# Performance work log

Measured on AMD Instinct MI355X. Metric: run time of the kernel, lower is better.

## Reference

```python
import jax, jax.numpy as jnp
from jax import lax
import numpy as np

B, S = 256, 512
VOCAB, EMB_D = 50000, 300
POS_MAX, POS_D = 512, 16
CNN_OUT, K, NCLASS = 50, 5, 10


def setup_inputs() -> dict:
    key = jax.random.key(0)
    ks = jax.random.split(key, 7)
    return {
        "tokens": jax.random.randint(ks[0], (B, S), 0, VOCAB),
        "embed_table": jax.random.normal(ks[1], (VOCAB, EMB_D), jnp.float32),
        "pos_table": jax.random.normal(ks[2], (POS_MAX, POS_D), jnp.float32),
        "conv_w": jax.random.normal(ks[3], (CNN_OUT, EMB_D + 2 * POS_D, K), jnp.float32) * 0.05,
        "conv_b": jax.random.normal(ks[4], (CNN_OUT,), jnp.float32) * 0.05,
        "fc_w": jax.random.normal(ks[5], (NCLASS, CNN_OUT), jnp.float32) * 0.1,
        "fc_b": jax.random.normal(ks[6], (NCLASS,), jnp.float32) * 0.1,
        "entity1": 1,
        "entity2": 2,
    }


def _nearest_entity_dist(tokens, entity, max_pos):
    # Distance from each token to the nearest occurrence of `entity`,
    # clipped to [0, max_pos-1]; sentences without the entity clip to max.
    Sl = tokens.shape[1]
    idx = jnp.arange(Sl)
    occ = tokens == entity  # [B, S]
    big = 2 * Sl
    # nearest occurrence index to the left (running max) and right (running min)
    left = lax.cummax(jnp.where(occ, idx, -big), axis=1)
    right = lax.cummin(jnp.where(occ, idx, big), axis=1, reverse=True)
    dist = jnp.minimum(idx - left, right - idx)
    return jnp.clip(dist, 0, max_pos - 1)


def reference(tokens, embed_table, pos_table, conv_w, conv_b, fc_w, fc_b,
              entity1, entity2):
    emb = embed_table[tokens]                      # [B, S, EMB_D] gather
    pad = jnp.all(emb == 0.0, axis=-1)             # [B, S] zero-row mask
    feats = [emb]
    for ent in (entity1, entity2):
        d = _nearest_entity_dist(tokens, ent, pos_table.shape[0])
        pe = pos_table[d]                          # [B, S, POS_D]
        pe = jnp.where(pad[..., None], 0.0, pe)    # zero masked positions
        feats.append(pe)
    x = jnp.concatenate(feats, axis=-1)            # [B, S, 332]
    x = jnp.transpose(x, (0, 2, 1))                # [B, C, S]
    pad_hw = conv_w.shape[-1] // 2
    y = lax.conv_general_dilated(
        x, conv_w, window_strides=(1,), padding=[(pad_hw, pad_hw)],
        dimension_numbers=("NCH", "OIH", "NCH"))
    y = jax.nn.relu(y + conv_b[None, :, None])     # [B, 50, S]
    y = jnp.max(y, axis=2)                         # full-length max pool -> [B, 50]
    out = y @ fc_w.T + fc_b                        # [B, NCLASS]
    return out
```

## Files before the change

kernel.cpp:

```cpp
#include <hip/hip_runtime.h>
#include <hip/hip_bf16.h>

typedef __attribute__((ext_vector_type(8))) short short8;
typedef __attribute__((ext_vector_type(4))) float floatx4;

#define BB 256
#define SS 512
#define VOCAB 50000
#define EMB_D 300
#define POS_MAX 512
#define POS_D 16
#define CNN_OUT 50
#define KW 5
#define NCLASS 10
#define C_IN 332
#define KS2 10
#define NB2 20
#define NWF2 (KS2 * NB2 * 64 * 8)
#define PSTR 320
#define ESTR 328
#define FSTR2 328
#define MTOK 32
#define MROWS 64
#define FROWS 68
#define NB_PACK 225
#define NB_POSP 640
#define NB_DIST BB

__device__ __forceinline__ unsigned pack2bf(float x, float y) {
    __hip_bfloat162 h = __float22bfloat162_rn(make_float2(x, y));
    return *reinterpret_cast<unsigned*>(&h);
}

__device__ __forceinline__ unsigned short f2bf(float x) {
    unsigned u = __float_as_uint(x);
    u += 0x7FFF + ((u >> 16) & 1);
    return (unsigned short)(u >> 16);
}

__device__ __forceinline__ float bflo(unsigned u) { return __uint_as_float(u << 16); }
__device__ __forceinline__ float bfhi(unsigned u) { return __uint_as_float(u & 0xFFFF0000u); }

__device__ __forceinline__ unsigned comb(unsigned a, unsigned b, unsigned c,
                                         float sa, float sp) {
    float rlo = sa * bflo(a) + sp * (bflo(b) + bflo(c));
    float rhi = sa * bfhi(a) + sp * (bfhi(b) + bfhi(c));
    return pack2bf(rlo, rhi);
}

__global__ __launch_bounds__(512) void k_prep(const float* __restrict__ conv_w,
                                              const float* __restrict__ pos,
                                              unsigned short* __restrict__ Wf2,
                                              unsigned short* __restrict__ P1,
                                              unsigned short* __restrict__ P2,
                                              float* __restrict__ ymax,
                                              const int* __restrict__ tokens,
                                              const int* __restrict__ e1p,
                                              const int* __restrict__ e2p,
                                              int* __restrict__ d1,
                                              int* __restrict__ d2) {
    __shared__ int cnt1, cnt2;
    __shared__ int lst1[SS], lst2[SS];
    int bid = blockIdx.x, tid = threadIdx.x;
    if (bid < NB_PACK) {
        int idx = bid * 512 + tid;
        if (idx < NWF2) {
            int j = idx & 7, l = (idx >> 3) & 63;
            int rest = idx >> 9;
            int nb = rest % 20, ks = rest / 20;
            int c = ks * 32 + ((l >> 4) << 3) + j;
            int col = nb * 16 + (l & 15);
            int k = col >> 6, o = col & 63;
            float v = 0.f;
            if (c < EMB_D && o < CNN_OUT)
                v = conv_w[o * (C_IN * KW) + c * KW + k];
            Wf2[idx] = f2bf(v);
        } else if (idx < NWF2 + BB * CNN_OUT) {
            ymax[idx - NWF2] = 0.f;
        }
    } else if (bid < NB_PACK + NB_POSP) {
        int idx = (bid - NB_PACK) * 512 + tid;
        int tb = idx / (POS_MAX * PSTR);
        int r = idx % (POS_MAX * PSTR);
        int d = r / PSTR, col = r % PSTR;
        int k = col >> 6, o = col & 63;
        float v = 0.f;
        if (o < CNN_OUT) {
            const float* pr = pos + d * POS_D;
            const float* wb = conv_w + o * (C_IN * KW) + (EMB_D + tb * POS_D) * KW + k;
            #pragma unroll
            for (int c = 0; c < POS_D; ++c) v += pr[c] * wb[c * KW];
        }
        (tb ? P2 : P1)[d * PSTR + col] = f2bf(v);
    } else {
        int b = bid - NB_PACK - NB_POSP;
        int s = tid;
        if (s == 0) { cnt1 = 0; cnt2 = 0; }
        __syncthreads();
        int tok = tokens[b * SS + s];
        int e1 = *e1p, e2 = *e2p;
        if (tok == e1) lst1[atomicAdd(&cnt1, 1)] = s;
        if (tok == e2) lst2[atomicAdd(&cnt2, 1)] = s;
        __syncthreads();
        int dd1 = POS_MAX - 1;
        int n1 = cnt1;
        for (int i = 0; i < n1; ++i) dd1 = min(dd1, abs(s - lst1[i]));
        int dd2 = POS_MAX - 1;
        int n2 = cnt2;
        for (int i = 0; i < n2; ++i) dd2 = min(dd2, abs(s - lst2[i]));
        d1[b * SS + s] = dd1;
        d2[b * SS + s] = dd2;
    }
}

__global__ __launch_bounds__(256, 2) void k_proj(const float* __restrict__ E,
                                                 const unsigned short* __restrict__ Wf2,
                                                 unsigned short* __restrict__ P,
                                                 int* __restrict__ rowz) {
    __shared__ __align__(16) unsigned short Elds[MTOK * ESTR];
    __shared__ int nzf[MTOK];
    int tid = threadIdx.x, lane = tid & 63, w = tid >> 6;
    int t0 = blockIdx.x * MTOK;

    if (tid < MTOK) nzf[tid] = 0;
    __syncthreads();

    float4 v[10];
    int vrow[10], vc4[10];
    bool vok[10];
    #pragma unroll
    for (int j = 0; j < 10; ++j) {
        int idx = tid + j * 256;
        vok[j] = (idx < MTOK * 75);
        int row = idx / 75, c4 = idx - row * 75;
        vrow[j] = row; vc4[j] = c4;
        int t = t0 + row;
        v[j] = (vok[j] && t < VOCAB)
             ? ((const float4*)(E + (size_t)t * EMB_D))[c4]
             : make_float4(0.f, 0.f, 0.f, 0.f);
    }
    #pragma unroll
    for (int j = 0; j < 10; ++j) {
        if (vok[j]) {
            bool nz = (v[j].x != 0.f) | (v[j].y != 0.f) | (v[j].z != 0.f) | (v[j].w != 0.f);
            if (nz) nzf[vrow[j]] = 1;
            *(uint2*)&Elds[vrow[j] * ESTR + vc4[j] * 4] =
                make_uint2(pack2bf(v[j].x, v[j].y), pack2bf(v[j].z, v[j].w));
        }
    }
    if (tid < MTOK * 5) {
        int row = tid / 5, u = tid - row * 5;
        *(uint2*)&Elds[row * ESTR + 300 + u * 4] = make_uint2(0u, 0u);
    }
    __syncthreads();

    if (tid < MTOK) {
        int t = t0 + tid;
        if (t < VOCAB) rowz[t] = nzf[tid] ? 0 : 1;
    }

    floatx4 acc[2][5];
    #pragma unroll
    for (int mm = 0; mm < 2; ++mm)
        #pragma unroll
        for (int nb = 0; nb < 5; ++nb) acc[mm][nb] = (floatx4)0.f;

    int arow = lane & 15, ach = (lane >> 4) * 8;
    const short8* Bp = (const short8*)Wf2;

    short8 bA[5], bB[5];
    #pragma unroll
    for (int nb = 0; nb < 5; ++nb)
        bA[nb] = Bp[(0 * NB2 + w * 5 + nb) * 64 + lane];
    #pragma unroll
    for (int nb = 0; nb < 5; ++nb)
        bB[nb] = Bp[(1 * NB2 + w * 5 + nb) * 64 + lane];

    auto step = [&](int ks, short8 (&bf)[5], int pfks) {
        short8 af[2];
        #pragma unroll
        for (int mm = 0; mm < 2; ++mm)
            af[mm] = *(const short8*)&Elds[(mm * 16 + arow) * ESTR + ks * 32 + ach];
        #pragma unroll
        for (int mm = 0; mm < 2; ++mm)
            #pragma unroll
            for (int nb = 0; nb < 5; ++nb)
                acc[mm][nb] = __builtin_amdgcn_mfma_f32_16x16x32_bf16(af[mm], bf[nb], acc[mm][nb], 0, 0, 0);
        if (pfks < KS2) {
            #pragma unroll
            for (int nb = 0; nb < 5; ++nb)
                bf[nb] = Bp[(pfks * NB2 + w * 5 + nb) * 64 + lane];
        }
    };

    #pragma unroll 1
    for (int ks = 0; ks < KS2; ks += 2) {
        step(ks, bA, ks + 2);
        step(ks + 1, bB, ks + 3);
    }

    __syncthreads();
    int drow = (lane >> 4) * 4, dcol = lane & 15;
    #pragma unroll
    for (int mm = 0; mm < 2; ++mm)
        #pragma unroll
        for (int nb = 0; nb < 5; ++nb)
            #pragma unroll
            for (int rg = 0; rg < 4; ++rg)
                Elds[(mm * 16 + drow + rg) * ESTR + (w * 5 + nb) * 16 + dcol] = f2bf(acc[mm][nb][rg]);
    __syncthreads();
    #pragma unroll
    for (int j = 0; j < 5; ++j) {
        int idx = tid + j * 256;
        int row = idx / 40, ch = idx - row * 40;
        int tt = t0 + row;
        if (tt < VOCAB)
            ((uint4*)P)[(size_t)tt * 40 + ch] = *(const uint4*)&Elds[row * ESTR + ch * 8];
    }
}

__global__ __launch_bounds__(512, 4) void k_conv(const int* __restrict__ tokens,
                                                 const int* __restrict__ d1,
                                                 const int* __restrict__ d2,
                                                 const int* __restrict__ rowz,
                                                 const unsigned short* __restrict__ P,
                                                 const unsigned short* __restrict__ P1,
                                                 const unsigned short* __restrict__ P2,
                                                 const float* __restrict__ conv_b,
                                                 float* __restrict__ ymax) {
    __shared__ __align__(16) unsigned short F[FROWS * FSTR2];
    __shared__ int td[FROWS], i1d[FROWS], i2d[FROWS];
    __shared__ float sad[FROWS], spd[FROWS];
    __shared__ float Rm[8][64];
    int tid = threadIdx.x, lane = tid & 63, w = tid >> 6;
    int b = blockIdx.x >> 3, sb = blockIdx.x & 7;
    int s0 = sb * MROWS;

    if (tid < FROWS) {
        int sp = s0 - 2 + tid;
        bool valid = (sp >= 0 && sp < SS);
        int t = valid ? tokens[b * SS + sp] : 0;
        td[tid] = t;
        i1d[tid] = valid ? d1[b * SS + sp] : 0;
        i2d[tid] = valid ? d2[b * SS + sp] : 0;
        sad[tid] = valid ? 1.f : 0.f;
        spd[tid] = (valid && !rowz[t]) ? 1.f : 0.f;
    }
    __syncthreads();

    const uint4* Pp  = (const uint4*)P;
    const uint4* P1p = (const uint4*)P1;
    const uint4* P2p = (const uint4*)P2;
    #pragma unroll
    for (int j = 0; j < 6; ++j) {
        int idx = tid + j * 512;
        if (idx < FROWS * 40) {
            int row = idx / 40, ch = idx % 40;
            uint4 a  = Pp[(size_t)td[row] * 40 + ch];
            uint4 bv = P1p[i1d[row] * 40 + ch];
            uint4 cv = P2p[i2d[row] * 40 + ch];
            float sa = sad[row], sp = spd[row];
            uint4 o;
            o.x = comb(a.x, bv.x, cv.x, sa, sp);
            o.y = comb(a.y, bv.y, cv.y, sa, sp);
            o.z = comb(a.z, bv.z, cv.z, sa, sp);
            o.w = comb(a.w, bv.w, cv.w, sa, sp);
            *(uint4*)&F[row * FSTR2 + ch * 8] = o;
        }
    }
    __syncthreads();

    int s = tid >> 3, og = (tid >> 1) & 3, h = tid & 1;
    float acc[8];
    #pragma unroll
    for (int i = 0; i < 8; ++i) acc[i] = 0.f;
    #pragma unroll
    for (int k = 0; k < KW; ++k) {
        uint4 v = *(const uint4*)&F[(s + k) * FSTR2 + k * 64 + og * 16 + h * 8];
        acc[0] += bflo(v.x); acc[1] += bfhi(v.x);
        acc[2] += bflo(v.y); acc[3] += bfhi(v.y);
        acc[4] += bflo(v.z); acc[5] += bfhi(v.z);
        acc[6] += bflo(v.w); acc[7] += bfhi(v.w);
    }
    #pragma unroll
    for (int i = 0; i < 8; ++i) {
        acc[i] = fmaxf(acc[i], __shfl_xor(acc[i], 8));
        acc[i] = fmaxf(acc[i], __shfl_xor(acc[i], 16));
        acc[i] = fmaxf(acc[i], __shfl_xor(acc[i], 32));
    }
    if ((lane & 56) == 0) {
        #pragma unroll
        for (int i = 0; i < 8; ++i)
            Rm[w][og * 16 + h * 8 + i] = acc[i];
    }
    __syncthreads();

    if (tid < CNN_OUT) {
        float mx = Rm[0][tid];
        #pragma unroll
        for (int w2 = 1; w2 < 8; ++w2) mx = fmaxf(mx, Rm[w2][tid]);
        mx = fmaxf(mx + conv_b[tid], 0.f);
        atomicMax((int*)ymax + b * CNN_OUT + tid, __float_as_int(mx));
    }
}

__global__ __launch_bounds__(64) void k_fc(const float* __restrict__ ymax,
                                           const float* __restrict__ fc_w,
                                           const float* __restrict__ fc_b,
                                           float* __restrict__ out) {
    int b = blockIdx.x, n = threadIdx.x;
    if (n < NCLASS) {
        float a = fc_b[n];
        #pragma unroll
        for (int o = 0; o < CNN_OUT; ++o)
            a += ymax[b * CNN_OUT + o] * fc_w[n * CNN_OUT + o];
        out[b * NCLASS + n] = a;
    }
}

extern "C" void kernel_launch(void* const* d_in, const int* in_sizes, int n_in,
                              void* d_out, int out_size, void* d_ws, size_t ws_size,
                              hipStream_t stream) {
    const int*   tokens  = (const int*)  d_in[0];
    const float* embed   = (const float*)d_in[1];
    const float* pos     = (const float*)d_in[2];
    const float* conv_w  = (const float*)d_in[3];
    const float* conv_b  = (const float*)d_in[4];
    const float* fc_w    = (const float*)d_in[5];
    const float* fc_b    = (const float*)d_in[6];
    const int*   e1p     = (const int*)  d_in[7];
    const int*   e2p     = (const int*)  d_in[8];
    float* out = (float*)d_out;

    char* ws = (char*)d_ws;
    size_t off = 0;
    unsigned short* P   = (unsigned short*)(ws + off); off += (size_t)VOCAB * PSTR * 2;
    unsigned short* Wf2 = (unsigned short*)(ws + off); off += (size_t)NWF2 * 2;
    unsigned short* P1  = (unsigned short*)(ws + off); off += (size_t)POS_MAX * PSTR * 2;
    unsigned short* P2  = (unsigned short*)(ws + off); off += (size_t)POS_MAX * PSTR * 2;
    int*   d1     = (int*)  (ws + off); off += (size_t)BB * SS * 4;
    int*   d2     = (int*)  (ws + off); off += (size_t)BB * SS * 4;
    int*   rowzp  = (int*)  (ws + off); off += (size_t)VOCAB * 4;
    float* ymax   = (float*)(ws + off); off += (size_t)BB * CNN_OUT * 4;
    (void)ws_size; (void)in_sizes; (void)n_in; (void)out_size;

    hipLaunchKernelGGL(k_prep, dim3(NB_PACK + NB_POSP + NB_DIST), dim3(512), 0, stream,
                       conv_w, pos, Wf2, P1, P2, ymax, tokens, e1p, e2p, d1, d2);
    hipLaunchKernelGGL(k_proj, dim3((VOCAB + MTOK - 1) / MTOK), dim3(256), 0, stream,
                       embed, Wf2, P, rowzp);
    hipLaunchKernelGGL(k_conv, dim3(BB * (SS / MROWS)), dim3(512), 0, stream,
                       tokens, d1, d2, rowzp, P, P1, P2, conv_b, ymax);
    hipLaunchKernelGGL(k_fc, dim3(BB), dim3(64), 0, stream, ymax, fc_w, fc_b, out);
}
```

Before: 60.76 us.

## Split weight packing out and merge projection, pos-table and distance work into one-wave blocks

Weight packing and the ymax zeroing move into a small standalone kernel. The vocab projection, the position-table precompute and the entity-distance computation are merged into a single kernel of 64-thread single-wave blocks. Each projection block now handles 16 tokens and loops over four output-column groups, staging results through a small scratch buffer before storing. The intent is to overlap the independent prep work with the projection and to raise block-level parallelism. The cost is that the A fragment is reloaded for each column group and each block carries less work, which can reduce data reuse.

```diff
diff --git a/kernel.cpp b/kernel.cpp
--- a/kernel.cpp
+++ b/kernel.cpp
@@ -20,10 +20,10 @@
 #define PSTR 320
 #define ESTR 328
 #define FSTR2 328
-#define MTOK 32
+#define MTOK 16
 #define MROWS 64
 #define FROWS 68
-#define NB_PACK 225
+#define NB_PROJ 3125
 #define NB_POSP 640
 #define NB_DIST BB
 
@@ -48,174 +48,165 @@
     return pack2bf(rlo, rhi);
 }
 
-__global__ __launch_bounds__(512) void k_prep(const float* __restrict__ conv_w,
+__global__ __launch_bounds__(256) void k_wf(const float* __restrict__ conv_w,
+                                            unsigned short* __restrict__ Wf2,
+                                            float* __restrict__ ymax) {
+    int idx = blockIdx.x * 256 + threadIdx.x;
+    if (idx < NWF2) {
+        int j = idx & 7, l = (idx >> 3) & 63;
+        int rest = idx >> 9;
+        int nb = rest % 20, ks = rest / 20;
+        int c = ks * 32 + ((l >> 4) << 3) + j;
+        int col = nb * 16 + (l & 15);
+        int k = col >> 6, o = col & 63;
+        float v = 0.f;
+        if (c < EMB_D && o < CNN_OUT)
+            v = conv_w[o * (C_IN * KW) + c * KW + k];
+        Wf2[idx] = f2bf(v);
+    } else if (idx < NWF2 + BB * CNN_OUT) {
+        ymax[idx - NWF2] = 0.f;
+    }
+}
+
+__global__ __launch_bounds__(64) void k_merge(const float* __restrict__ E,
+                                              const unsigned short* __restrict__ Wf2,
+                                              unsigned short* __restrict__ P,
+                                              int* __restrict__ rowz,
+                                              const float* __restrict__ conv_w,
                                               const float* __restrict__ pos,
-                                              unsigned short* __restrict__ Wf2,
                                               unsigned short* __restrict__ P1,
                                               unsigned short* __restrict__ P2,
-                                              float* __restrict__ ymax,
                                               const int* __restrict__ tokens,
                                               const int* __restrict__ e1p,
                                               const int* __restrict__ e2p,
                                               int* __restrict__ d1,
                                               int* __restrict__ d2) {
-    __shared__ int cnt1, cnt2;
-    __shared__ int lst1[SS], lst2[SS];
-    int bid = blockIdx.x, tid = threadIdx.x;
-    if (bid < NB_PACK) {
-        int idx = bid * 512 + tid;
-        if (idx < NWF2) {
-            int j = idx & 7, l = (idx >> 3) & 63;
-            int rest = idx >> 9;
-            int nb = rest % 20, ks = rest / 20;
-            int c = ks * 32 + ((l >> 4) << 3) + j;
-            int col = nb * 16 + (l & 15);
+    __shared__ __align__(16) char smem[13248];
+    int bid = blockIdx.x, lane = threadIdx.x;
+
+    if (bid < NB_PROJ) {
+        unsigned short* Elds = (unsigned short*)smem;
+        unsigned short* Sc   = (unsigned short*)(smem + 10496);
+        int* nzf             = (int*)(smem + 13056);
+        int t0 = bid * MTOK;
+
+        if (lane < MTOK) nzf[lane] = 0;
+        #pragma unroll
+        for (int j = 0; j < 19; ++j) {
+            int idx = lane + j * 64;
+            if (idx < MTOK * 75) {
+                int row = idx / 75, c4 = idx - row * 75;
+                float4 v = ((const float4*)(E + (size_t)(t0 + row) * EMB_D))[c4];
+                if ((v.x != 0.f) | (v.y != 0.f) | (v.z != 0.f) | (v.w != 0.f)) nzf[row] = 1;
+                *(uint2*)&Elds[row * ESTR + c4 * 4] =
+                    make_uint2(pack2bf(v.x, v.y), pack2bf(v.z, v.w));
+            }
+        }
+        #pragma unroll
+        for (int j = 0; j < 2; ++j) {
+            int idx = lane + j * 64;
+            if (idx < MTOK * 5) {
+                int row = idx / 5, u = idx - row * 5;
+                *(uint2*)&Elds[row * ESTR + 300 + u * 4] = make_uint2(0u, 0u);
+            }
+        }
+        if (lane < MTOK) rowz[t0 + lane] = nzf[lane] ? 0 : 1;
+
+        int arow = lane & 15, ach = (lane >> 4) * 8;
+        int drow = (lane >> 4) * 4, dcol = lane & 15;
+        const short8* Bp = (const short8*)Wf2;
+        #pragma unroll 1
+        for (int g = 0; g < 4; ++g) {
+            floatx4 acc[5];
+            #pragma unroll
+            for (int nb = 0; nb < 5; ++nb) acc[nb] = (floatx4)0.f;
+            short8 bA[5], bB[5];
+            #pragma unroll
+            for (int nb = 0; nb < 5; ++nb)
+                bA[nb] = Bp[(0 * NB2 + g * 5 + nb) * 64 + lane];
+            #pragma unroll
+            for (int nb = 0; nb < 5; ++nb)
+                bB[nb] = Bp[(1 * NB2 + g * 5 + nb) * 64 + lane];
+            #pragma unroll 1
+            for (int ks = 0; ks < KS2; ks += 2) {
+                short8 af = *(const short8*)&Elds[arow * ESTR + ks * 32 + ach];
+                #pragma unroll
+                for (int nb = 0; nb < 5; ++nb)
+                    acc[nb] = __builtin_amdgcn_mfma_f32_16x16x32_bf16(af, bA[nb], acc[nb], 0, 0, 0);
+                if (ks + 2 < KS2)
+                    #pragma unroll
+                    for (int nb = 0; nb < 5; ++nb)
+                        bA[nb] = Bp[((ks + 2) * NB2 + g * 5 + nb) * 64 + lane];
+                short8 af2 = *(const short8*)&Elds[arow * ESTR + (ks + 1) * 32 + ach];
+                #pragma unroll
+                for (int nb = 0; nb < 5; ++nb)
+                    acc[nb] = __builtin_amdgcn_mfma_f32_16x16x32_bf16(af2, bB[nb], acc[nb], 0, 0, 0);
+                if (ks + 3 < KS2)
+                    #pragma unroll
+                    for (int nb = 0; nb < 5; ++nb)
+                        bB[nb] = Bp[((ks + 3) * NB2 + g * 5 + nb) * 64 + lane];
+            }
+            #pragma unroll
+            for (int nb = 0; nb < 5; ++nb)
+                #pragma unroll
+                for (int rg = 0; rg < 4; ++rg)
+                    Sc[(drow + rg) * 80 + nb * 16 + dcol] = f2bf(acc[nb][rg]);
+            #pragma unroll
+            for (int j = 0; j < 3; ++j) {
+                int idx = lane + j * 64;
+                if (idx < 160) {
+                    int row = idx / 10, ch = idx - row * 10;
+                    ((uint4*)P)[(size_t)(t0 + row) * 40 + g * 10 + ch] =
+                        *(const uint4*)&Sc[row * 80 + ch * 8];
+                }
+            }
+        }
+    } else if (bid < NB_PROJ + NB_POSP) {
+        int base = (bid - NB_PROJ) * 512;
+        #pragma unroll 1
+        for (int j = 0; j < 8; ++j) {
+            int idx = base + lane + j * 64;
+            int tb = idx / (POS_MAX * PSTR);
+            int r = idx % (POS_MAX * PSTR);
+            int d = r / PSTR, col = r % PSTR;
             int k = col >> 6, o = col & 63;
             float v = 0.f;
-            if (c < EMB_D && o < CNN_OUT)
-                v = conv_w[o * (C_IN * KW) + c * KW + k];
-            Wf2[idx] = f2bf(v);
-        } else if (idx < NWF2 + BB * CNN_OUT) {
-            ymax[idx - NWF2] = 0.f;
-        }
-    } else if (bid < NB_PACK + NB_POSP) {
-        int idx = (bid - NB_PACK) * 512 + tid;
-        int tb = idx / (POS_MAX * PSTR);
-        int r = idx % (POS_MAX * PSTR);
-        int d = r / PSTR, col = r % PSTR;
-        int k = col >> 6, o = col & 63;
-        float v = 0.f;
-        if (o < CNN_OUT) {
-            const float* pr = pos + d * POS_D;
-            const float* wb = conv_w + o * (C_IN * KW) + (EMB_D + tb * POS_D) * KW + k;
-            #pragma unroll
-            for (int c = 0; c < POS_D; ++c) v += pr[c] * wb[c * KW];
-        }
-        (tb ? P2 : P1)[d * PSTR + col] = f2bf(v);
+            if (o < CNN_OUT) {
+                const float* pr = pos + d * POS_D;
+                const float* wb = conv_w + o * (C_IN * KW) + (EMB_D + tb * POS_D) * KW + k;
+                #pragma unroll
+                for (int c = 0; c < POS_D; ++c) v += pr[c] * wb[c * KW];
+            }
+            (tb ? P2 : P1)[d * PSTR + col] = f2bf(v);
+        }
     } else {
-        int b = bid - NB_PACK - NB_POSP;
-        int s = tid;
-        if (s == 0) { cnt1 = 0; cnt2 = 0; }
+        int* lst1 = (int*)smem;
+        int* lst2 = (int*)(smem + 2048);
+        int* cnts = (int*)(smem + 4096);
+        int b = bid - NB_PROJ - NB_POSP;
+        if (lane < 2) cnts[lane] = 0;
         __syncthreads();
-        int tok = tokens[b * SS + s];
         int e1 = *e1p, e2 = *e2p;
-        if (tok == e1) lst1[atomicAdd(&cnt1, 1)] = s;
-        if (tok == e2) lst2[atomicAdd(&cnt2, 1)] = s;
+        int toks[8];
+        #pragma unroll
+        for (int j = 0; j < 8; ++j) {
+            int s = lane + j * 64;
+            toks[j] = tokens[b * SS + s];
+            if (toks[j] == e1) lst1[atomicAdd(&cnts[0], 1)] = s;
+            if (toks[j] == e2) lst2[atomicAdd(&cnts[1], 1)] = s;
+        }
         __syncthreads();
-        int dd1 = POS_MAX - 1;
-        int n1 = cnt1;
-        for (int i = 0; i < n1; ++i) dd1 = min(dd1, abs(s - lst1[i]));
-        int dd2 = POS_MAX - 1;
-        int n2 = cnt2;
-        for (int i = 0; i < n2; ++i) dd2 = min(dd2, abs(s - lst2[i]));
-        d1[b * SS + s] = dd1;
-        d2[b * SS + s] = dd2;
-    }
-}
-
-__global__ __launch_bounds__(256, 2) void k_proj(const float* __restrict__ E,
-                                                 const unsigned short* __restrict__ Wf2,
-                                                 unsigned short* __restrict__ P,
-                                                 int* __restrict__ rowz) {
-    __shared__ __align__(16) unsigned short Elds[MTOK * ESTR];
-    __shared__ int nzf[MTOK];
-    int tid = threadIdx.x, lane = tid & 63, w = tid >> 6;
-    int t0 = blockIdx.x * MTOK;
-
-    if (tid < MTOK) nzf[tid] = 0;
-    __syncthreads();
-
-    float4 v[10];
-    int vrow[10], vc4[10];
-    bool vok[10];
-    #pragma unroll
-    for (int j = 0; j < 10; ++j) {
-        int idx = tid + j * 256;
-        vok[j] = (idx < MTOK * 75);
-        int row = idx / 75, c4 = idx - row * 75;
-        vrow[j] = row; vc4[j] = c4;
-        int t = t0 + row;
-        v[j] = (vok[j] && t < VOCAB)
-             ? ((const float4*)(E + (size_t)t * EMB_D))[c4]
-             : make_float4(0.f, 0.f, 0.f, 0.f);
-    }
-    #pragma unroll
-    for (int j = 0; j < 10; ++j) {
-        if (vok[j]) {
-            bool nz = (v[j].x != 0.f) | (v[j].y != 0.f) | (v[j].z != 0.f) | (v[j].w != 0.f);
-            if (nz) nzf[vrow[j]] = 1;
-            *(uint2*)&Elds[vrow[j] * ESTR + vc4[j] * 4] =
-                make_uint2(pack2bf(v[j].x, v[j].y), pack2bf(v[j].z, v[j].w));
-        }
-    }
-    if (tid < MTOK * 5) {
-        int row = tid / 5, u = tid - row * 5;
-        *(uint2*)&Elds[row * ESTR + 300 + u * 4] = make_uint2(0u, 0u);
-    }
-    __syncthreads();
-
-    if (tid < MTOK) {
-        int t = t0 + tid;
-        if (t < VOCAB) rowz[t] = nzf[tid] ? 0 : 1;
-    }
-
-    floatx4 acc[2][5];
-    #pragma unroll
-    for (int mm = 0; mm < 2; ++mm)
-        #pragma unroll
-        for (int nb = 0; nb < 5; ++nb) acc[mm][nb] = (floatx4)0.f;
-
-    int arow = lane & 15, ach = (lane >> 4) * 8;
-    const short8* Bp = (const short8*)Wf2;
-
-    short8 bA[5], bB[5];
-    #pragma unroll
-    for (int nb = 0; nb < 5; ++nb)
-        bA[nb] = Bp[(0 * NB2 + w * 5 + nb) * 64 + lane];
-    #pragma unroll
-    for (int nb = 0; nb < 5; ++nb)
-        bB[nb] = Bp[(1 * NB2 + w * 5 + nb) * 64 + lane];
-
-    auto step = [&](int ks, short8 (&bf)[5], int pfks) {
-        short8 af[2];
-        #pragma unroll
-        for (int mm = 0; mm < 2; ++mm)
-            af[mm] = *(const short8*)&Elds[(mm * 16 + arow) * ESTR + ks * 32 + ach];
-        #pragma unroll
-        for (int mm = 0; mm < 2; ++mm)
-            #pragma unroll
-            for (int nb = 0; nb < 5; ++nb)
-                acc[mm][nb] = __builtin_amdgcn_mfma_f32_16x16x32_bf16(af[mm], bf[nb], acc[mm][nb], 0, 0, 0);
-        if (pfks < KS2) {
-            #pragma unroll
-            for (int nb = 0; nb < 5; ++nb)
-                bf[nb] = Bp[(pfks * NB2 + w * 5 + nb) * 64 + lane];
-        }
-    };
-
-    #pragma unroll 1
-    for (int ks = 0; ks < KS2; ks += 2) {
-        step(ks, bA, ks + 2);
-        step(ks + 1, bB, ks + 3);
-    }
-
-    __syncthreads();
-    int drow = (lane >> 4) * 4, dcol = lane & 15;
-    #pragma unroll
-    for (int mm = 0; mm < 2; ++mm)
-        #pragma unroll
-        for (int nb = 0; nb < 5; ++nb)
-            #pragma unroll
-            for (int rg = 0; rg < 4; ++rg)
-                Elds[(mm * 16 + drow + rg) * ESTR + (w * 5 + nb) * 16 + dcol] = f2bf(acc[mm][nb][rg]);
-    __syncthreads();
-    #pragma unroll
-    for (int j = 0; j < 5; ++j) {
-        int idx = tid + j * 256;
-        int row = idx / 40, ch = idx - row * 40;
-        int tt = t0 + row;
-        if (tt < VOCAB)
-            ((uint4*)P)[(size_t)tt * 40 + ch] = *(const uint4*)&Elds[row * ESTR + ch * 8];
+        int n1 = cnts[0], n2 = cnts[1];
+        #pragma unroll 1
+        for (int j = 0; j < 8; ++j) {
+            int s = lane + j * 64;
+            int dd1 = POS_MAX - 1;
+            for (int i = 0; i < n1; ++i) dd1 = min(dd1, abs(s - lst1[i]));
+            int dd2 = POS_MAX - 1;
+            for (int i = 0; i < n2; ++i) dd2 = min(dd2, abs(s - lst2[i]));
+            d1[b * SS + s] = dd1;
+            d2[b * SS + s] = dd2;
+        }
     }
 }
 
@@ -344,10 +335,10 @@
     float* ymax   = (float*)(ws + off); off += (size_t)BB * CNN_OUT * 4;
     (void)ws_size; (void)in_sizes; (void)n_in; (void)out_size;
 
-    hipLaunchKernelGGL(k_prep, dim3(NB_PACK + NB_POSP + NB_DIST), dim3(512), 0, stream,
-                       conv_w, pos, Wf2, P1, P2, ymax, tokens, e1p, e2p, d1, d2);
-    hipLaunchKernelGGL(k_proj, dim3((VOCAB + MTOK - 1) / MTOK), dim3(256), 0, stream,
-                       embed, Wf2, P, rowzp);
+    hipLaunchKernelGGL(k_wf, dim3((NWF2 + BB * CNN_OUT + 255) / 256), dim3(256), 0, stream,
+                       conv_w, Wf2, ymax);
+    hipLaunchKernelGGL(k_merge, dim3(NB_PROJ + NB_POSP + NB_DIST), dim3(64), 0, stream,
+                       embed, Wf2, P, rowzp, conv_w, pos, P1, P2, tokens, e1p, e2p, d1, d2);
     hipLaunchKernelGGL(k_conv, dim3(BB * (SS / MROWS)), dim3(512), 0, stream,
                        tokens, d1, d2, rowzp, P, P1, P2, conv_b, ymax);
     hipLaunchKernelGGL(k_fc, dim3(BB), dim3(64), 0, stream, ymax, fc_w, fc_b, out);
```

Result: slower. 76.86 us (+26.5%).

## Move pos-projection and distance work into projection kernel, split weight packing out

Applied to the files above, without the earlier changes.

Restructures the prep stages. Weight packing and ymax zeroing move into a small standalone kernel. The position-table projection and entity-distance computation move into the same launch as the vocabulary projection GEMM, as extra block ranges sharing one shared-memory buffer. The aim is for the small independent tasks to run alongside the large projection instead of serialising in a separate launch ahead of it. In exchange, those blocks now run at 256 threads with the projection's launch bounds and shared-memory footprint, and the weight packing still runs as its own serial launch first.

```diff
diff --git a/kernel.cpp b/kernel.cpp
--- a/kernel.cpp
+++ b/kernel.cpp
@@ -23,8 +23,8 @@
 #define MTOK 32
 #define MROWS 64
 #define FROWS 68
-#define NB_PACK 225
-#define NB_POSP 640
+#define NB_PROJ 1563
+#define NB_POSP 1280
 #define NB_DIST BB
 
 __device__ __forceinline__ unsigned pack2bf(float x, float y) {
@@ -48,38 +48,145 @@
     return pack2bf(rlo, rhi);
 }
 
-__global__ __launch_bounds__(512) void k_prep(const float* __restrict__ conv_w,
-                                              const float* __restrict__ pos,
-                                              unsigned short* __restrict__ Wf2,
-                                              unsigned short* __restrict__ P1,
-                                              unsigned short* __restrict__ P2,
-                                              float* __restrict__ ymax,
-                                              const int* __restrict__ tokens,
-                                              const int* __restrict__ e1p,
-                                              const int* __restrict__ e2p,
-                                              int* __restrict__ d1,
-                                              int* __restrict__ d2) {
-    __shared__ int cnt1, cnt2;
-    __shared__ int lst1[SS], lst2[SS];
+__global__ __launch_bounds__(256) void k_wf(const float* __restrict__ conv_w,
+                                            unsigned short* __restrict__ Wf2,
+                                            float* __restrict__ ymax) {
+    int idx = blockIdx.x * 256 + threadIdx.x;
+    if (idx < NWF2) {
+        int j = idx & 7, l = (idx >> 3) & 63;
+        int rest = idx >> 9;
+        int nb = rest % 20, ks = rest / 20;
+        int c = ks * 32 + ((l >> 4) << 3) + j;
+        int col = nb * 16 + (l & 15);
+        int k = col >> 6, o = col & 63;
+        float v = 0.f;
+        if (c < EMB_D && o < CNN_OUT)
+            v = conv_w[o * (C_IN * KW) + c * KW + k];
+        Wf2[idx] = f2bf(v);
+    } else if (idx < NWF2 + BB * CNN_OUT) {
+        ymax[idx - NWF2] = 0.f;
+    }
+}
+
+__global__ __launch_bounds__(256, 2) void k_projm(const float* __restrict__ E,
+                                                  const unsigned short* __restrict__ Wf2,
+                                                  unsigned short* __restrict__ P,
+                                                  int* __restrict__ rowz,
+                                                  const float* __restrict__ conv_w,
+                                                  const float* __restrict__ pos,
+                                                  unsigned short* __restrict__ P1,
+                                                  unsigned short* __restrict__ P2,
+                                                  const int* __restrict__ tokens,
+                                                  const int* __restrict__ e1p,
+                                                  const int* __restrict__ e2p,
+                                                  int* __restrict__ d1,
+                                                  int* __restrict__ d2) {
+    __shared__ __align__(16) char smem[21120];
     int bid = blockIdx.x, tid = threadIdx.x;
-    if (bid < NB_PACK) {
-        int idx = bid * 512 + tid;
-        if (idx < NWF2) {
-            int j = idx & 7, l = (idx >> 3) & 63;
-            int rest = idx >> 9;
-            int nb = rest % 20, ks = rest / 20;
-            int c = ks * 32 + ((l >> 4) << 3) + j;
-            int col = nb * 16 + (l & 15);
-            int k = col >> 6, o = col & 63;
-            float v = 0.f;
-            if (c < EMB_D && o < CNN_OUT)
-                v = conv_w[o * (C_IN * KW) + c * KW + k];
-            Wf2[idx] = f2bf(v);
-        } else if (idx < NWF2 + BB * CNN_OUT) {
-            ymax[idx - NWF2] = 0.f;
-        }
-    } else if (bid < NB_PACK + NB_POSP) {
-        int idx = (bid - NB_PACK) * 512 + tid;
+
+    if (bid < NB_PROJ) {
+        unsigned short* Elds = (unsigned short*)smem;
+        int* nzf = (int*)(smem + 20992);
+        int lane = tid & 63, w = tid >> 6;
+        int t0 = bid * MTOK;
+
+        if (tid < MTOK) nzf[tid] = 0;
+        __syncthreads();
+
+        float4 v[10];
+        int vrow[10], vc4[10];
+        bool vok[10];
+        #pragma unroll
+        for (int j = 0; j < 10; ++j) {
+            int idx = tid + j * 256;
+            vok[j] = (idx < MTOK * 75);
+            int row = idx / 75, c4 = idx - row * 75;
+            vrow[j] = row; vc4[j] = c4;
+            int t = t0 + row;
+            v[j] = (vok[j] && t < VOCAB)
+                 ? ((const float4*)(E + (size_t)t * EMB_D))[c4]
+                 : make_float4(0.f, 0.f, 0.f, 0.f);
+        }
+        #pragma unroll
+        for (int j = 0; j < 10; ++j) {
+            if (vok[j]) {
+                bool nz = (v[j].x != 0.f) | (v[j].y != 0.f) | (v[j].z != 0.f) | (v[j].w != 0.f);
+                if (nz) nzf[vrow[j]] = 1;
+                *(uint2*)&Elds[vrow[j] * ESTR + vc4[j] * 4] =
+                    make_uint2(pack2bf(v[j].x, v[j].y), pack2bf(v[j].z, v[j].w));
+            }
+        }
+        if (tid < MTOK * 5) {
+            int row = tid / 5, u = tid - row * 5;
+            *(uint2*)&Elds[row * ESTR + 300 + u * 4] = make_uint2(0u, 0u);
+        }
+        __syncthreads();
+
+        if (tid < MTOK) {
+            int t = t0 + tid;
+            if (t < VOCAB) rowz[t] = nzf[tid] ? 0 : 1;
+        }
+
+        floatx4 acc[2][5];
+        #pragma unroll
+        for (int mm = 0; mm < 2; ++mm)
+            #pragma unroll
+            for (int nb = 0; nb < 5; ++nb) acc[mm][nb] = (floatx4)0.f;
+
+        int arow = lane & 15, ach = (lane >> 4) * 8;
+        const short8* Bp = (const short8*)Wf2;
+
+        short8 bA[5], bB[5];
+        #pragma unroll
+        for (int nb = 0; nb < 5; ++nb)
+            bA[nb] = Bp[(0 * NB2 + w * 5 + nb) * 64 + lane];
+        #pragma unroll
+        for (int nb = 0; nb < 5; ++nb)
+            bB[nb] = Bp[(1 * NB2 + w * 5 + nb) * 64 + lane];
+
+        auto step = [&](int ks, short8 (&bf)[5], int pfks) {
+            short8 af[2];
+            #pragma unroll
+            for (int mm = 0; mm < 2; ++mm)
+                af[mm] = *(const short8*)&Elds[(mm * 16 + arow) * ESTR + ks * 32 + ach];
+            #pragma unroll
+            for (int mm = 0; mm < 2; ++mm)
+                #pragma unroll
+                for (int nb = 0; nb < 5; ++nb)
+                    acc[mm][nb] = __builtin_amdgcn_mfma_f32_16x16x32_bf16(af[mm], bf[nb], acc[mm][nb], 0, 0, 0);
+            if (pfks < KS2) {
+                #pragma unroll
+                for (int nb = 0; nb < 5; ++nb)
+                    bf[nb] = Bp[(pfks * NB2 + w * 5 + nb) * 64 + lane];
+            }
+        };
+
+        #pragma unroll 1
+        for (int ks = 0; ks < KS2; ks += 2) {
+            step(ks, bA, ks + 2);
+            step(ks + 1, bB, ks + 3);
+        }
+
+        __syncthreads();
+        int drow = (lane >> 4) * 4, dcol = lane & 15;
+        #pragma unroll
+        for (int mm = 0; mm < 2; ++mm)
+            #pragma unroll
+            for (int nb = 0; nb < 5; ++nb)
+                #pragma unroll
+                for (int rg = 0; rg < 4; ++rg)
+                    Elds[(mm * 16 + drow + rg) * ESTR + (w * 5 + nb) * 16 + dcol] = f2bf(acc[mm][nb][rg]);
+        __syncthreads();
+        #pragma unroll
+        for (int j = 0; j < 5; ++j) {
+            int idx = tid + j * 256;
+            int row = idx / 40, ch = idx - row * 40;
+            int tt = t0 + row;
+            if (tt < VOCAB)
+                ((uint4*)P)[(size_t)tt * 40 + ch] = *(const uint4*)&Elds[row * ESTR + ch * 8];
+        }
+    } else if (bid < NB_PROJ + NB_POSP) {
+        int idx = (bid - NB_PROJ) * 256 + tid;
         int tb = idx / (POS_MAX * PSTR);
         int r = idx % (POS_MAX * PSTR);
         int d = r / PSTR, col = r % PSTR;
@@ -93,129 +200,32 @@
         }
         (tb ? P2 : P1)[d * PSTR + col] = f2bf(v);
     } else {
-        int b = bid - NB_PACK - NB_POSP;
-        int s = tid;
-        if (s == 0) { cnt1 = 0; cnt2 = 0; }
-        __syncthreads();
-        int tok = tokens[b * SS + s];
+        int* lst1 = (int*)smem;
+        int* lst2 = (int*)(smem + 2048);
+        int* cnts = (int*)(smem + 4096);
+        int b = bid - NB_PROJ - NB_POSP;
+        if (tid < 2) cnts[tid] = 0;
+        __syncthreads();
         int e1 = *e1p, e2 = *e2p;
-        if (tok == e1) lst1[atomicAdd(&cnt1, 1)] = s;
-        if (tok == e2) lst2[atomicAdd(&cnt2, 1)] = s;
-        __syncthreads();
-        int dd1 = POS_MAX - 1;
-        int n1 = cnt1;
-        for (int i = 0; i < n1; ++i) dd1 = min(dd1, abs(s - lst1[i]));
-        int dd2 = POS_MAX - 1;
-        int n2 = cnt2;
-        for (int i = 0; i < n2; ++i) dd2 = min(dd2, abs(s - lst2[i]));
-        d1[b * SS + s] = dd1;
-        d2[b * SS + s] = dd2;
-    }
-}
-
-__global__ __launch_bounds__(256, 2) void k_proj(const float* __restrict__ E,
-                                                 const unsigned short* __restrict__ Wf2,
-                                                 unsigned short* __restrict__ P,
-                                                 int* __restrict__ rowz) {
-    __shared__ __align__(16) unsigned short Elds[MTOK * ESTR];
-    __shared__ int nzf[MTOK];
-    int tid = threadIdx.x, lane = tid & 63, w = tid >> 6;
-    int t0 = blockIdx.x * MTOK;
-
-    if (tid < MTOK) nzf[tid] = 0;
-    __syncthreads();
-
-    float4 v[10];
-    int vrow[10], vc4[10];
-    bool vok[10];
-    #pragma unroll
-    for (int j = 0; j < 10; ++j) {
-        int idx = tid + j * 256;
-        vok[j] = (idx < MTOK * 75);
-        int row = idx / 75, c4 = idx - row * 75;
-        vrow[j] = row; vc4[j] = c4;
-        int t = t0 + row;
-        v[j] = (vok[j] && t < VOCAB)
-             ? ((const float4*)(E + (size_t)t * EMB_D))[c4]
-             : make_float4(0.f, 0.f, 0.f, 0.f);
-    }
-    #pragma unroll
-    for (int j = 0; j < 10; ++j) {
-        if (vok[j]) {
-            bool nz = (v[j].x != 0.f) | (v[j].y != 0.f) | (v[j].z != 0.f) | (v[j].w != 0.f);
-            if (nz) nzf[vrow[j]] = 1;
-            *(uint2*)&Elds[vrow[j] * ESTR + vc4[j] * 4] =
-                make_uint2(pack2bf(v[j].x, v[j].y), pack2bf(v[j].z, v[j].w));
-        }
-    }
-    if (tid < MTOK * 5) {
-        int row = tid / 5, u = tid - row * 5;
-        *(uint2*)&Elds[row * ESTR + 300 + u * 4] = make_uint2(0u, 0u);
-    }
-    __syncthreads();
-
-    if (tid < MTOK) {
-        int t = t0 + tid;
-        if (t < VOCAB) rowz[t] = nzf[tid] ? 0 : 1;
-    }
-
-    floatx4 acc[2][5];
-    #pragma unroll
-    for (int mm = 0; mm < 2; ++mm)
-        #pragma unroll
-        for (int nb = 0; nb < 5; ++nb) acc[mm][nb] = (floatx4)0.f;
-
-    int arow = lane & 15, ach = (lane >> 4) * 8;
-    const short8* Bp = (const short8*)Wf2;
-
-    short8 bA[5], bB[5];
-    #pragma unroll
-    for (int nb = 0; nb < 5; ++nb)
-        bA[nb] = Bp[(0 * NB2 + w * 5 + nb) * 64 + lane];
-    #pragma unroll
-    for (int nb = 0; nb < 5; ++nb)
-        bB[nb] = Bp[(1 * NB2 + w * 5 + nb) * 64 + lane];
-
-    auto step = [&](int ks, short8 (&bf)[5], int pfks) {
-        short8 af[2];
-        #pragma unroll
-        for (int mm = 0; mm < 2; ++mm)
-            af[mm] = *(const short8*)&Elds[(mm * 16 + arow) * ESTR + ks * 32 + ach];
-        #pragma unroll
-        for (int mm = 0; mm < 2; ++mm)
-            #pragma unroll
-            for (int nb = 0; nb < 5; ++nb)
-                acc[mm][nb] = __builtin_amdgcn_mfma_f32_16x16x32_bf16(af[mm], bf[nb], acc[mm][nb], 0, 0, 0);
-        if (pfks < KS2) {
-            #pragma unroll
-            for (int nb = 0; nb < 5; ++nb)
-                bf[nb] = Bp[(pfks * NB2 + w * 5 + nb) * 64 + lane];
-        }
-    };
-
-    #pragma unroll 1
-    for (int ks = 0; ks < KS2; ks += 2) {
-        step(ks, bA, ks + 2);
-        step(ks + 1, bB, ks + 3);
-    }
-
-    __syncthreads();
-    int drow = (lane >> 4) * 4, dcol = lane & 15;
-    #pragma unroll
-    for (int mm = 0; mm < 2; ++mm)
-        #pragma unroll
-        for (int nb = 0; nb < 5; ++nb)
-            #pragma unroll
-            for (int rg = 0; rg < 4; ++rg)
-                Elds[(mm * 16 + drow + rg) * ESTR + (w * 5 + nb) * 16 + dcol] = f2bf(acc[mm][nb][rg]);
-    __syncthreads();
-    #pragma unroll
-    for (int j = 0; j < 5; ++j) {
-        int idx = tid + j * 256;
-        int row = idx / 40, ch = idx - row * 40;
-        int tt = t0 + row;
-        if (tt < VOCAB)
-            ((uint4*)P)[(size_t)tt * 40 + ch] = *(const uint4*)&Elds[row * ESTR + ch * 8];
+        #pragma unroll
+        for (int j = 0; j < 2; ++j) {
+            int s = tid + j * 256;
+            int tok = tokens[b * SS + s];
+            if (tok == e1) lst1[atomicAdd(&cnts[0], 1)] = s;
+            if (tok == e2) lst2[atomicAdd(&cnts[1], 1)] = s;
+        }
+        __syncthreads();
+        int n1 = cnts[0], n2 = cnts[1];
+        #pragma unroll 1
+        for (int j = 0; j < 2; ++j) {
+            int s = tid + j * 256;
+            int dd1 = POS_MAX - 1;
+            for (int i = 0; i < n1; ++i) dd1 = min(dd1, abs(s - lst1[i]));
+            int dd2 = POS_MAX - 1;
+            for (int i = 0; i < n2; ++i) dd2 = min(dd2, abs(s - lst2[i]));
+            d1[b * SS + s] = dd1;
+            d2[b * SS + s] = dd2;
+        }
     }
 }
 
@@ -344,10 +354,10 @@
     float* ymax   = (float*)(ws + off); off += (size_t)BB * CNN_OUT * 4;
     (void)ws_size; (void)in_sizes; (void)n_in; (void)out_size;
 
-    hipLaunchKernelGGL(k_prep, dim3(NB_PACK + NB_POSP + NB_DIST), dim3(512), 0, stream,
-                       conv_w, pos, Wf2, P1, P2, ymax, tokens, e1p, e2p, d1, d2);
-    hipLaunchKernelGGL(k_proj, dim3((VOCAB + MTOK - 1) / MTOK), dim3(256), 0, stream,
-                       embed, Wf2, P, rowzp);
+    hipLaunchKernelGGL(k_wf, dim3((NWF2 + BB * CNN_OUT + 255) / 256), dim3(256), 0, stream,
+                       conv_w, Wf2, ymax);
+    hipLaunchKernelGGL(k_projm, dim3(NB_PROJ + NB_POSP + NB_DIST), dim3(256), 0, stream,
+                       embed, Wf2, P, rowzp, conv_w, pos, P1, P2, tokens, e1p, e2p, d1, d2);
     hipLaunchKernelGGL(k_conv, dim3(BB * (SS / MROWS)), dim3(512), 0, stream,
                        tokens, d1, d2, rowzp, P, P1, P2, conv_b, ymax);
     hipLaunchKernelGGL(k_fc, dim3(BB), dim3(64), 0, stream, ymax, fc_w, fc_b, out);
```

New measurement: 60.59 us. About the same (-0.3%).
